# Kernel tuning notes

Measured on AMD Instinct MI355X. Metric: run time of the kernel, lower is better.

## Reference

```python
import jax, jax.numpy as jnp
import numpy as np

B, L, D, C, H, M = 256, 500, 3, 32, 512, 5
I = D + C            # per-step input dim (dihedrals concat condition)
O = D * M            # out_dim * num_mixtures


def setup_inputs() -> dict:
    key = jax.random.key(0)
    ks = jax.random.split(key, 6)
    return {
        "inputs": jax.random.normal(ks[0], (B, L, D), dtype=jnp.float32),
        "z": jax.random.normal(ks[1], (B, L, C), dtype=jnp.float32),
        "W_enc": jax.random.normal(ks[2], (L, I, H), dtype=jnp.float32),
        "b_enc": jnp.zeros((1, H), dtype=jnp.float32),
        "V_mu": jax.random.normal(ks[3], (L, H, O), dtype=jnp.float32),
        "b_mu": jnp.zeros((L, 1, O), dtype=jnp.float32),
        "V_sigma": jax.random.normal(ks[4], (L, H, O), dtype=jnp.float32),
        "b_sigma": jnp.zeros((L, 1, O), dtype=jnp.float32),
        "V_pi": jax.random.normal(ks[5], (L, H, M), dtype=jnp.float32),
        "b_pi": jnp.zeros((L, 1, M), dtype=jnp.float32),
    }


def reference(inputs, z, W_enc, b_enc, V_mu, b_mu, V_sigma, b_sigma, V_pi, b_pi):
    # x: [L, B, I]
    x = jnp.transpose(jnp.concatenate([inputs, z], axis=2), (1, 0, 2))
    # per-step contributions c[i] = x[i] @ W_enc[i] -> [L, B, H]
    c = jnp.einsum('lbi,lih->lbh', x, W_enc)
    # a[i] = b_enc + sum_{j<i} c[j]  (exclusive prefix sum of the recurrence)
    csum = jnp.cumsum(c, axis=0)
    a = jnp.concatenate([jnp.zeros_like(csum[:1]), csum[:-1]], axis=0) + b_enc
    h = jax.nn.relu(a)  # [L, B, H]
    h_mu = jnp.einsum('lbh,lho->lbo', h, V_mu) + b_mu        # [L, B, O]
    h_sigma = jnp.einsum('lbh,lho->lbo', h, V_sigma) + b_sigma
    h_pi = jnp.einsum('lbh,lhm->lbm', h, V_pi) + b_pi        # [L, B, M]
    logits = jnp.concatenate([h_mu, h_sigma, h_pi], axis=2)  # [L, B, 2O+M]
    return jnp.transpose(logits, (1, 0, 2))                  # [B, L, 2O+M]
```

## Files before the change

kernel.cpp:

```cpp
#include <hip/hip_runtime.h>

constexpr int B = 256, L = 500, D = 3, C = 32, I = 35, H = 512, O = 15, M = 5;
constexpr int KP1 = 48;
constexpr int JP = 48;
constexpr int KPV = 520;
constexpr int G = 100;
constexpr int LC = 5;

typedef __attribute__((ext_vector_type(8))) _Float16 half8;
typedef __attribute__((ext_vector_type(2))) _Float16 half2;
typedef __attribute__((ext_vector_type(16))) float f32x16;

__global__ __launch_bounds__(256) void k0x(const float* __restrict__ inp,
                                           const float* __restrict__ z,
                                           _Float16* __restrict__ xT) {
  const int l = blockIdx.x, tid = threadIdx.x;
  __shared__ _Float16 xs[B][38];
  const float* ip = inp + ((size_t)tid * L + l) * D;
  const float4* zp = (const float4*)(z + ((size_t)tid * L + l) * C);
  xs[tid][0] = (_Float16)ip[0];
  xs[tid][1] = (_Float16)ip[1];
  xs[tid][2] = (_Float16)ip[2];
#pragma unroll
  for (int q = 0; q < 8; ++q) {
    float4 v = zp[q];
    xs[tid][D + q * 4 + 0] = (_Float16)v.x;
    xs[tid][D + q * 4 + 1] = (_Float16)v.y;
    xs[tid][D + q * 4 + 2] = (_Float16)v.z;
    xs[tid][D + q * 4 + 3] = (_Float16)v.w;
  }
  __syncthreads();
  unsigned int* dst = (unsigned int*)(xT + (size_t)l * B * KP1);
  for (int f = tid; f < B * (KP1 / 2); f += 256) {
    int b = f / (KP1 / 2), k = (f - b * (KP1 / 2)) * 2;
    unsigned int lo = (k < I)     ? *(const unsigned short*)&xs[b][k]     : 0u;
    unsigned int hi = (k + 1 < I) ? *(const unsigned short*)&xs[b][k + 1] : 0u;
    dst[f] = lo | (hi << 16);
  }
}

__global__ __launch_bounds__(256) void k0w(const float* __restrict__ W,
                                           _Float16* __restrict__ Wt) {
  const int l = blockIdx.x, tid = threadIdx.x;
  __shared__ _Float16 ws[H][37];
  for (int f = tid; f < I * H; f += 256) {
    int i = f >> 9, h = f & 511;
    ws[h][i] = (_Float16)W[((size_t)l * I + i) * H + h];
  }
  __syncthreads();
  unsigned int* dst = (unsigned int*)(Wt + (size_t)l * H * KP1);
  for (int f = tid; f < H * (KP1 / 2); f += 256) {
    int h = f / (KP1 / 2), k = (f - h * (KP1 / 2)) * 2;
    unsigned int lo = (k < I)     ? *(const unsigned short*)&ws[h][k]     : 0u;
    unsigned int hi = (k + 1 < I) ? *(const unsigned short*)&ws[h][k + 1] : 0u;
    dst[f] = lo | (hi << 16);
  }
}

__global__ __launch_bounds__(256) void k0v(const float* __restrict__ Vmu,
                                           const float* __restrict__ Vsg,
                                           const float* __restrict__ Vpi,
                                           _Float16* __restrict__ Vt) {
  const int l = blockIdx.x, tid = threadIdx.x;
  __shared__ __align__(16) _Float16 Vs[JP * KPV];
  for (int f = tid; f < (JP * KPV) / 8; f += 256) ((uint4*)Vs)[f] = (uint4){0, 0, 0, 0};
  __syncthreads();
  const float* vm = Vmu + (size_t)l * H * O;
  const float* vs = Vsg + (size_t)l * H * O;
  const float* vp = Vpi + (size_t)l * H * M;
  for (int idx = tid; idx < H * O; idx += 256) {
    int k = idx / O, j = idx - k * O;
    Vs[j * KPV + k]       = (_Float16)vm[idx];
    Vs[(O + j) * KPV + k] = (_Float16)vs[idx];
  }
  for (int idx = tid; idx < H * M; idx += 256) {
    int k = idx / M, j = idx - k * M;
    Vs[(2 * O + j) * KPV + k] = (_Float16)vp[idx];
  }
  __syncthreads();
  uint4* dst = (uint4*)(Vt + (size_t)l * JP * KPV);
  for (int f = tid; f < (JP * KPV) / 8; f += 256) dst[f] = ((const uint4*)Vs)[f];
}

__global__ __launch_bounds__(256, 3) void kA(const _Float16* __restrict__ xT,
                                             const _Float16* __restrict__ Wt,
                                             _Float16* __restrict__ S) {
  const int idx = blockIdx.x;
  const int g = ((idx >> 6) << 3) + (idx & 7);
  if (g >= G) return;
  const int b0 = ((idx >> 3) & 7) * 32;
  const int w = threadIdx.x >> 6, lane = threadIdx.x & 63;
  const int ln31 = lane & 31, hi32 = lane >> 5;

  f32x16 acc[4];
#pragma unroll
  for (int mt = 0; mt < 4; ++mt)
#pragma unroll
    for (int r = 0; r < 16; ++r) acc[mt][r] = 0.f;

#pragma unroll 1
  for (int t = 0; t < LC; ++t) {
    const int l = g * LC + t;
    const _Float16* Xb = xT + ((size_t)l * B + b0 + ln31) * KP1 + 8 * hi32;
    const _Float16* Wb = Wt + ((size_t)l * H + 128 * w + ln31) * KP1 + 8 * hi32;
    half8 xf[3], wf[12];
#pragma unroll
    for (int kt = 0; kt < 3; ++kt) xf[kt] = *(const half8*)(Xb + 16 * kt);
#pragma unroll
    for (int mt = 0; mt < 4; ++mt)
#pragma unroll
      for (int kt = 0; kt < 3; ++kt)
        wf[mt * 3 + kt] = *(const half8*)(Wb + (size_t)mt * 32 * KP1 + 16 * kt);
#pragma unroll
    for (int mt = 0; mt < 4; ++mt)
#pragma unroll
      for (int kt = 0; kt < 3; ++kt)
        acc[mt] = __builtin_amdgcn_mfma_f32_32x32x16_f16(wf[mt * 3 + kt], xf[kt], acc[mt], 0, 0, 0);
  }
  _Float16* Sp = S + ((size_t)g * H + 128 * w) * B + b0 + ln31;
#pragma unroll
  for (int mt = 0; mt < 4; ++mt)
#pragma unroll
    for (int r = 0; r < 16; ++r) {
      const int hl = 32 * mt + (r & 3) + 8 * (r >> 2) + 4 * hi32;
      Sp[(size_t)hl * B] = (_Float16)acc[mt][r];
    }
}

__global__ __launch_bounds__(256) void kS(const _Float16* __restrict__ S,
                                          const float* __restrict__ benc,
                                          _Float16* __restrict__ Acc) {
  const int t = blockIdx.x * 256 + threadIdx.x;
  const int b = t & (B - 1), h = t >> 8;
  float run = benc[h];
  const _Float16* sp = S + (size_t)h * B + b;
  _Float16* ap = Acc + (size_t)h * B + b;
  constexpr size_t stride = (size_t)H * B;
#pragma unroll 5
  for (int g = 0; g < G; ++g) {
    ap[g * stride] = (_Float16)run;
    run += (float)sp[g * stride];
  }
}

__global__ __launch_bounds__(256, 2) void kB(const _Float16* __restrict__ xT,
                                             const _Float16* __restrict__ Wt,
                                             const _Float16* __restrict__ Vt,
                                             const _Float16* __restrict__ Acc,
                                             const float* __restrict__ bmu,
                                             const float* __restrict__ bsg,
                                             const float* __restrict__ bpi,
                                             float* __restrict__ out) {
  const int idx = blockIdx.x;
  const int g = ((idx >> 6) << 3) + (idx & 7);
  if (g >= G) return;
  const int b0 = ((idx >> 3) & 7) * 32;
  const int tid = threadIdx.x;
  const int w = tid >> 6, lane = tid & 63;
  const int ln31 = lane & 31, hi32 = lane >> 5;

  __shared__ _Float16 po[4][LC][32][36];
  __shared__ float bias_s[LC][35];

  if (tid < LC * 35) {
    const int t = tid / 35, j = tid - 35 * t, l = g * LC + t;
    bias_s[t][j] = (j < O) ? bmu[l * O + j]
                 : (j < 2 * O) ? bsg[l * O + (j - O)]
                 : bpi[l * M + (j - 2 * O)];
  }

  f32x16 acc[4];
  const _Float16* Ap = Acc + ((size_t)g * H + 128 * w) * B + b0 + ln31;
#pragma unroll
  for (int mt = 0; mt < 4; ++mt)
#pragma unroll
    for (int r = 0; r < 16; ++r) {
      const int hl = 32 * mt + (r & 3) + 8 * (r >> 2) + 4 * hi32;
      acc[mt][r] = (float)Ap[(size_t)hl * B];
    }

#pragma unroll 1
  for (int t = 0; t < LC; ++t) {
    const int l = g * LC + t;
    const _Float16* Vb = Vt + (size_t)l * JP * KPV + 128 * w + 8 * hi32;
    half8 va0[8];
#pragma unroll
    for (int s = 0; s < 8; ++s)
      va0[s] = *(const half8*)(Vb + 16 * s + (size_t)ln31 * KPV);
    half8 va1[8];
#pragma unroll
    for (int s = 0; s < 8; ++s) {
      va1[s] = half8{};
      if (ln31 < 3)
        va1[s] = *(const half8*)(Vb + 16 * s + (size_t)(32 + ln31) * KPV);
    }
    half8 xf[3], wf[12];
    if (t != LC - 1) {
      const _Float16* Xb = xT + ((size_t)l * B + b0 + ln31) * KP1 + 8 * hi32;
      const _Float16* Wb = Wt + ((size_t)l * H + 128 * w + ln31) * KP1 + 8 * hi32;
#pragma unroll
      for (int kt = 0; kt < 3; ++kt) xf[kt] = *(const half8*)(Xb + 16 * kt);
#pragma unroll
      for (int mt = 0; mt < 4; ++mt)
#pragma unroll
        for (int kt = 0; kt < 3; ++kt)
          wf[mt * 3 + kt] = *(const half8*)(Wb + (size_t)mt * 32 * KP1 + 16 * kt);
    }
    f32x16 o0, o1;
#pragma unroll
    for (int r = 0; r < 16; ++r) { o0[r] = 0.f; o1[r] = 0.f; }
#pragma unroll
    for (int mt = 0; mt < 4; ++mt) {
      unsigned P0[4], P1[4];
#pragma unroll
      for (int m = 0; m < 4; ++m) {
        float e0 = fmaxf(acc[mt][4 * m + 0], 0.f);
        float e1 = fmaxf(acc[mt][4 * m + 1], 0.f);
        float e2 = fmaxf(acc[mt][4 * m + 2], 0.f);
        float e3 = fmaxf(acc[mt][4 * m + 3], 0.f);
        P0[m] = __builtin_bit_cast(unsigned, __builtin_amdgcn_cvt_pkrtz(e0, e1));
        P1[m] = __builtin_bit_cast(unsigned, __builtin_amdgcn_cvt_pkrtz(e2, e3));
      }
#pragma unroll
      for (int tl = 0; tl < 2; ++tl) {
        unsigned w0 = P0[2 * tl], w2 = P0[2 * tl + 1];
        unsigned w1 = P1[2 * tl], w3 = P1[2 * tl + 1];
        asm("v_permlane32_swap_b32 %0, %1" : "+v"(w0), "+v"(w2));
        asm("v_permlane32_swap_b32 %0, %1" : "+v"(w1), "+v"(w3));
        half2 a0 = __builtin_bit_cast(half2, w0);
        half2 a1 = __builtin_bit_cast(half2, w1);
        half2 a2 = __builtin_bit_cast(half2, w2);
        half2 a3 = __builtin_bit_cast(half2, w3);
        half8 hb = {a0.x, a0.y, a1.x, a1.y, a2.x, a2.y, a3.x, a3.y};
        o0 = __builtin_amdgcn_mfma_f32_32x32x16_f16(va0[2 * mt + tl], hb, o0, 0, 0, 0);
        o1 = __builtin_amdgcn_mfma_f32_32x32x16_f16(va1[2 * mt + tl], hb, o1, 0, 0, 0);
      }
    }
    _Float16* pw = &po[w][t][ln31][0];
#pragma unroll
    for (int r = 0; r < 16; r += 2) {
      const int j0 = (r & 3) + 8 * (r >> 2) + 4 * hi32;
      *(unsigned*)&pw[j0] =
          __builtin_bit_cast(unsigned, __builtin_amdgcn_cvt_pkrtz(o0[r], o0[r + 1]));
    }
    if (hi32 == 0) {
      *(unsigned*)&pw[32] =
          __builtin_bit_cast(unsigned, __builtin_amdgcn_cvt_pkrtz(o1[0], o1[1]));
      pw[34] = (_Float16)o1[2];
    }
    if (t != LC - 1) {
#pragma unroll
      for (int mt = 0; mt < 4; ++mt)
#pragma unroll
        for (int kt = 0; kt < 3; ++kt)
          acc[mt] = __builtin_amdgcn_mfma_f32_32x32x16_f16(wf[mt * 3 + kt], xf[kt], acc[mt], 0, 0, 0);
    }
  }
  __syncthreads();
  for (int f = tid; f < 32 * LC * 35; f += 256) {
    const int b = f / (LC * 35);
    const int r = f - b * (LC * 35);
    const int t = r / 35, j = r - 35 * t;
    const float s = (float)po[0][t][b][j] + (float)po[1][t][b][j] +
                    (float)po[2][t][b][j] + (float)po[3][t][b][j];
    out[((size_t)(b0 + b) * L + g * LC + t) * 35 + j] = s + bias_s[t][j];
  }
}

extern "C" void kernel_launch(void* const* d_in, const int* in_sizes, int n_in,
                              void* d_out, int out_size, void* d_ws, size_t ws_size,
                              hipStream_t stream) {
  const float* inp  = (const float*)d_in[0];
  const float* z    = (const float*)d_in[1];
  const float* Wenc = (const float*)d_in[2];
  const float* benc = (const float*)d_in[3];
  const float* Vmu  = (const float*)d_in[4];
  const float* bmu  = (const float*)d_in[5];
  const float* Vsg  = (const float*)d_in[6];
  const float* bsg  = (const float*)d_in[7];
  const float* Vpi  = (const float*)d_in[8];
  const float* bpi  = (const float*)d_in[9];
  float* out = (float*)d_out;

  char* ws = (char*)d_ws;
  _Float16* xT  = (_Float16*)ws;
  _Float16* Wt  = (_Float16*)(ws + 12288000);
  _Float16* Vt  = (_Float16*)(ws + 36864000);
  _Float16* S   = (_Float16*)(ws + 61824000);
  _Float16* Acc = (_Float16*)(ws + 88038400);

  k0x<<<dim3(L), 256, 0, stream>>>(inp, z, xT);
  k0w<<<dim3(L), 256, 0, stream>>>(Wenc, Wt);
  k0v<<<dim3(L), 256, 0, stream>>>(Vmu, Vsg, Vpi, Vt);
  kA<<<dim3(832), 256, 0, stream>>>(xT, Wt, S);
  kS<<<dim3(B * H / 256), 256, 0, stream>>>(S, benc, Acc);
  kB<<<dim3(832), 256, 0, stream>>>(xT, Wt, Vt, Acc, bmu, bsg, bpi, out);
}
```

Measured before the change: 252.2 us.

## Merge three prep kernels into one launch with register-based fp16 packing

Combines the x, W and V conversion kernels into a single kPrep launch with 3*L blocks, picking the role by block index. The x and W paths now convert in registers using packed round-toward-zero fp16 conversion and write 16-byte vector stores, instead of going through a shared-memory transpose. The kA timestep loop is also fully unrolled. The goal is to cut launch overhead and shared-memory traffic in the prep stage, at the cost of more registers and of every block reserving the large V shared buffer, which may lower occupancy.

```diff
diff --git a/kernel.cpp b/kernel.cpp
--- a/kernel.cpp
+++ b/kernel.cpp
@@ -11,75 +11,79 @@
 typedef __attribute__((ext_vector_type(2))) _Float16 half2;
 typedef __attribute__((ext_vector_type(16))) float f32x16;
 
-__global__ __launch_bounds__(256) void k0x(const float* __restrict__ inp,
-                                           const float* __restrict__ z,
-                                           _Float16* __restrict__ xT) {
-  const int l = blockIdx.x, tid = threadIdx.x;
-  __shared__ _Float16 xs[B][38];
-  const float* ip = inp + ((size_t)tid * L + l) * D;
-  const float4* zp = (const float4*)(z + ((size_t)tid * L + l) * C);
-  xs[tid][0] = (_Float16)ip[0];
-  xs[tid][1] = (_Float16)ip[1];
-  xs[tid][2] = (_Float16)ip[2];
-#pragma unroll
-  for (int q = 0; q < 8; ++q) {
-    float4 v = zp[q];
-    xs[tid][D + q * 4 + 0] = (_Float16)v.x;
-    xs[tid][D + q * 4 + 1] = (_Float16)v.y;
-    xs[tid][D + q * 4 + 2] = (_Float16)v.z;
-    xs[tid][D + q * 4 + 3] = (_Float16)v.w;
-  }
-  __syncthreads();
-  unsigned int* dst = (unsigned int*)(xT + (size_t)l * B * KP1);
-  for (int f = tid; f < B * (KP1 / 2); f += 256) {
-    int b = f / (KP1 / 2), k = (f - b * (KP1 / 2)) * 2;
-    unsigned int lo = (k < I)     ? *(const unsigned short*)&xs[b][k]     : 0u;
-    unsigned int hi = (k + 1 < I) ? *(const unsigned short*)&xs[b][k + 1] : 0u;
-    dst[f] = lo | (hi << 16);
-  }
-}
-
-__global__ __launch_bounds__(256) void k0w(const float* __restrict__ W,
-                                           _Float16* __restrict__ Wt) {
-  const int l = blockIdx.x, tid = threadIdx.x;
-  __shared__ _Float16 ws[H][37];
-  for (int f = tid; f < I * H; f += 256) {
-    int i = f >> 9, h = f & 511;
-    ws[h][i] = (_Float16)W[((size_t)l * I + i) * H + h];
-  }
-  __syncthreads();
-  unsigned int* dst = (unsigned int*)(Wt + (size_t)l * H * KP1);
-  for (int f = tid; f < H * (KP1 / 2); f += 256) {
-    int h = f / (KP1 / 2), k = (f - h * (KP1 / 2)) * 2;
-    unsigned int lo = (k < I)     ? *(const unsigned short*)&ws[h][k]     : 0u;
-    unsigned int hi = (k + 1 < I) ? *(const unsigned short*)&ws[h][k + 1] : 0u;
-    dst[f] = lo | (hi << 16);
-  }
-}
-
-__global__ __launch_bounds__(256) void k0v(const float* __restrict__ Vmu,
-                                           const float* __restrict__ Vsg,
-                                           const float* __restrict__ Vpi,
-                                           _Float16* __restrict__ Vt) {
-  const int l = blockIdx.x, tid = threadIdx.x;
+__global__ __launch_bounds__(256) void kPrep(const float* __restrict__ inp,
+                                             const float* __restrict__ z,
+                                             const float* __restrict__ W,
+                                             const float* __restrict__ Vmu,
+                                             const float* __restrict__ Vsg,
+                                             const float* __restrict__ Vpi,
+                                             _Float16* __restrict__ xT,
+                                             _Float16* __restrict__ Wt,
+                                             _Float16* __restrict__ Vt) {
+  const int bx = blockIdx.x, tid = threadIdx.x;
   __shared__ __align__(16) _Float16 Vs[JP * KPV];
-  for (int f = tid; f < (JP * KPV) / 8; f += 256) ((uint4*)Vs)[f] = (uint4){0, 0, 0, 0};
-  __syncthreads();
-  const float* vm = Vmu + (size_t)l * H * O;
-  const float* vs = Vsg + (size_t)l * H * O;
-  const float* vp = Vpi + (size_t)l * H * M;
-  for (int idx = tid; idx < H * O; idx += 256) {
-    int k = idx / O, j = idx - k * O;
-    Vs[j * KPV + k]       = (_Float16)vm[idx];
-    Vs[(O + j) * KPV + k] = (_Float16)vs[idx];
-  }
-  for (int idx = tid; idx < H * M; idx += 256) {
-    int k = idx / M, j = idx - k * M;
-    Vs[(2 * O + j) * KPV + k] = (_Float16)vp[idx];
-  }
-  __syncthreads();
-  uint4* dst = (uint4*)(Vt + (size_t)l * JP * KPV);
-  for (int f = tid; f < (JP * KPV) / 8; f += 256) dst[f] = ((const uint4*)Vs)[f];
+
+  if (bx < L) {
+    const int l = bx, b = tid;
+    float e[36];
+    const float* ip = inp + ((size_t)b * L + l) * D;
+    e[0] = ip[0]; e[1] = ip[1]; e[2] = ip[2];
+    const float4* zp = (const float4*)(z + ((size_t)b * L + l) * C);
+#pragma unroll
+    for (int q = 0; q < 8; ++q) {
+      float4 v = zp[q];
+      e[D + 4 * q + 0] = v.x; e[D + 4 * q + 1] = v.y;
+      e[D + 4 * q + 2] = v.z; e[D + 4 * q + 3] = v.w;
+    }
+    e[35] = 0.f;
+    unsigned u[24];
+#pragma unroll
+    for (int q = 0; q < 18; ++q)
+      u[q] = __builtin_bit_cast(unsigned, __builtin_amdgcn_cvt_pkrtz(e[2 * q], e[2 * q + 1]));
+#pragma unroll
+    for (int q = 18; q < 24; ++q) u[q] = 0u;
+    uint4* dst = (uint4*)(xT + ((size_t)l * B + b) * KP1);
+#pragma unroll
+    for (int q = 0; q < 6; ++q) dst[q] = ((const uint4*)u)[q];
+  } else if (bx < 2 * L) {
+    const int l = bx - L;
+#pragma unroll
+    for (int hp = 0; hp < 2; ++hp) {
+      const int h = tid + 256 * hp;
+      float v[36];
+#pragma unroll
+      for (int i = 0; i < I; ++i) v[i] = W[((size_t)l * I + i) * H + h];
+      v[35] = 0.f;
+      unsigned u[24];
+#pragma unroll
+      for (int q = 0; q < 18; ++q)
+        u[q] = __builtin_bit_cast(unsigned, __builtin_amdgcn_cvt_pkrtz(v[2 * q], v[2 * q + 1]));
+#pragma unroll
+      for (int q = 18; q < 24; ++q) u[q] = 0u;
+      uint4* dst = (uint4*)(Wt + ((size_t)l * H + h) * KP1);
+#pragma unroll
+      for (int q = 0; q < 6; ++q) dst[q] = ((const uint4*)u)[q];
+    }
+  } else {
+    const int l = bx - 2 * L;
+    for (int f = tid; f < (JP * KPV) / 8; f += 256) ((uint4*)Vs)[f] = (uint4){0, 0, 0, 0};
+    __syncthreads();
+    const float* vm = Vmu + (size_t)l * H * O;
+    const float* vs = Vsg + (size_t)l * H * O;
+    const float* vp = Vpi + (size_t)l * H * M;
+    for (int idx = tid; idx < H * O; idx += 256) {
+      int k = idx / O, j = idx - k * O;
+      Vs[j * KPV + k]       = (_Float16)vm[idx];
+      Vs[(O + j) * KPV + k] = (_Float16)vs[idx];
+    }
+    for (int idx = tid; idx < H * M; idx += 256) {
+      int k = idx / M, j = idx - k * M;
+      Vs[(2 * O + j) * KPV + k] = (_Float16)vp[idx];
+    }
+    __syncthreads();
+    uint4* dst = (uint4*)(Vt + (size_t)l * JP * KPV);
+    for (int f = tid; f < (JP * KPV) / 8; f += 256) dst[f] = ((const uint4*)Vs)[f];
+  }
 }
 
 __global__ __launch_bounds__(256, 3) void kA(const _Float16* __restrict__ xT,
@@ -98,7 +102,7 @@
 #pragma unroll
     for (int r = 0; r < 16; ++r) acc[mt][r] = 0.f;
 
-#pragma unroll 1
+#pragma unroll
   for (int t = 0; t < LC; ++t) {
     const int l = g * LC + t;
     const _Float16* Xb = xT + ((size_t)l * B + b0 + ln31) * KP1 + 8 * hi32;
@@ -289,9 +293,7 @@
   _Float16* S   = (_Float16*)(ws + 61824000);
   _Float16* Acc = (_Float16*)(ws + 88038400);
 
-  k0x<<<dim3(L), 256, 0, stream>>>(inp, z, xT);
-  k0w<<<dim3(L), 256, 0, stream>>>(Wenc, Wt);
-  k0v<<<dim3(L), 256, 0, stream>>>(Vmu, Vsg, Vpi, Vt);
+  kPrep<<<dim3(3 * L), 256, 0, stream>>>(inp, z, Wenc, Vmu, Vsg, Vpi, xT, Wt, Vt);
   kA<<<dim3(832), 256, 0, stream>>>(xT, Wt, S);
   kS<<<dim3(B * H / 256), 256, 0, stream>>>(S, benc, Acc);
   kB<<<dim3(832), 256, 0, stream>>>(xT, Wt, Vt, Acc, bmu, bsg, bpi, out);
```

Measured after the change: 238.8 us. 1.06x faster.
